# Optimization experiments

Hardware: AMD Instinct MI355X
Metric: run time of the kernel (lower is better)

Reference implementation:

```python
import jax, jax.numpy as jnp
import numpy as np

EPS = 1e-3  # keras LayerNormalization default epsilon


def layer_norm(x, gamma, beta):
    mean = jnp.mean(x, axis=-1, keepdims=True)
    var = jnp.var(x, axis=-1, keepdims=True)
    return (x - mean) * jax.lax.rsqrt(var + EPS) * gamma + beta


def setup_inputs() -> dict:
    key = jax.random.key(0)
    ks = jax.random.split(key, 4)
    B, H, W, C, Ci = 16, 64, 64, 512, 64
    return {
        "x": jax.random.normal(ks[0], (B, H, W, C), dtype=jnp.float32),
        "Wf": jax.random.normal(ks[1], (C, Ci), dtype=jnp.float32) * (1.0 / np.sqrt(C)),
        "Wh": jax.random.normal(ks[2], (C, Ci), dtype=jnp.float32) * (1.0 / np.sqrt(C)),
        "Wfgh": jax.random.normal(ks[3], (Ci, C), dtype=jnp.float32) * (1.0 / np.sqrt(Ci)),
        "gamma_f": jnp.ones((Ci,), jnp.float32),
        "beta_f": jnp.zeros((Ci,), jnp.float32),
        "gamma_h": jnp.ones((Ci,), jnp.float32),
        "beta_h": jnp.zeros((Ci,), jnp.float32),
        "gamma_fgh": jnp.ones((C,), jnp.float32),
        "beta_fgh": jnp.zeros((C,), jnp.float32),
        "scale": jnp.ones((1,), jnp.float32),
    }


def reference(x, Wf, Wh, Wfgh, gamma_f, beta_f, gamma_h, beta_h, gamma_fgh, beta_fgh, scale):
    # NOTE: original code uses w_f / LN_f for BOTH f and g branches (w_g unused).
    fg_base = layer_norm(jnp.einsum("bhwc,cd->bhwd", x, Wf), gamma_f, beta_f)  # [B,H,W,Ci]
    f = jnp.transpose(fg_base, (0, 2, 1, 3))  # Permute(2,1,3): swap H and W
    g = fg_base
    h = layer_norm(jnp.einsum("bhwc,cd->bhwd", x, Wh), gamma_h, beta_h)
    attn = jax.nn.softmax(f * g, axis=1)  # softmax over height axis
    out = jnp.einsum("bhwd,dc->bhwc", attn * h, Wfgh)
    out = layer_norm(out, gamma_fgh, beta_fgh)
    return out * scale + x
```

## Files before the change

### kernel.cpp

```cpp
#include <hip/hip_runtime.h>
#include <math.h>

#define BB 16
#define HH 64
#define WW 64
#define CC 512
#define CI 64
#define NROWS (BB * HH * WW)
#define LN_EPS 1e-3f

typedef __attribute__((ext_vector_type(8))) short bf16x8;
typedef __attribute__((ext_vector_type(4))) float f32x4;

__device__ __forceinline__ unsigned short f2bf(float f) {
  union {
    float f;
    unsigned int u;
  } v;
  v.f = f;
  unsigned int r = v.u + 0x7FFF + ((v.u >> 16) & 1);
  return (unsigned short)(r >> 16);
}

__device__ __forceinline__ float bf2f(unsigned short u) {
  union {
    unsigned int u;
    float f;
  } v;
  v.u = ((unsigned int)u) << 16;
  return v.f;
}

__device__ __forceinline__ unsigned int cvt_pk_bf16(float a, float b) {
  unsigned int r;
  asm("v_cvt_pk_bf16_f32 %0, %1, %2" : "=v"(r) : "v"(a), "v"(b));
  return r;
}

__device__ __forceinline__ void gload_lds16(const float* g, float* l) {
  __builtin_amdgcn_global_load_lds(
      (const __attribute__((address_space(1))) void*)g,
      (__attribute__((address_space(3))) void*)l, 16, 0, 0);
}

__global__ __launch_bounds__(256) void sgsa_prep(
    const float* __restrict__ Wf, const float* __restrict__ Wh,
    const float* __restrict__ Wo, unsigned short* __restrict__ WcT,
    unsigned short* __restrict__ WoT) {
  int tid = blockIdx.x * 256 + threadIdx.x;
  for (int i = tid; i < 128 * 512; i += gridDim.x * 256) {
    int col = i >> 9, k = i & 511;
    float v = (col < 64) ? Wf[k * 64 + col] : Wh[k * 64 + (col - 64)];
    WcT[i] = f2bf(v);
  }
  for (int i = tid; i < 512 * 64; i += gridDim.x * 256) {
    int col = i >> 6, k = i & 63;
    WoT[i] = f2bf(Wo[k * 512 + col]);
  }
}

__global__ __launch_bounds__(128) void sgsa_k1_mfma(
    const float* __restrict__ x, const unsigned short* __restrict__ WcT,
    const float* __restrict__ gf, const float* __restrict__ bf,
    const float* __restrict__ gh, const float* __restrict__ bh,
    float* __restrict__ fg, float* __restrict__ hl) {
  __shared__ float lds_a[2][64 * 64];

  const int tid = threadIdx.x;
  const int lane = tid & 63;
  const int wv = tid >> 6;
  const int cq = lane & 15;
  const int kg = lane >> 4;
  const int brow0 = blockIdx.x * 64;

  f32x4 acc[2][8];
#pragma unroll
  for (int rt = 0; rt < 2; ++rt)
#pragma unroll
    for (int ct = 0; ct < 8; ++ct) acc[rt][ct] = (f32x4){0.f, 0.f, 0.f, 0.f};

  int s_row[8], s_chk[8];
#pragma unroll
  for (int i = 0; i < 8; ++i) {
    int lin = (wv * 8 + i) * 64 + lane;
    s_row[i] = lin >> 4;
    s_chk[i] = (lin & 15) ^ ((lin >> 4) & 15);
  }

  auto stage = [&](int bufp, int ks) {
#pragma unroll
    for (int i = 0; i < 8; ++i) {
      const float* src =
          &x[(size_t)(brow0 + s_row[i]) * CC + ks * 64 + s_chk[i] * 4];
      gload_lds16(src, &lds_a[bufp][(wv * 8 + i) * 256]);
    }
  };

  stage(0, 0);
  __syncthreads();

  for (int ks = 0; ks < 8; ++ks) {
    const int bufp = ks & 1;
    if (ks < 7) stage(bufp ^ 1, ks + 1);

    const int kb0 = ks * 64;
#pragma unroll
    for (int kh = 0; kh < 2; ++kh) {
      const int kb2 = kh * 32;
      bf16x8 bfr[8];
#pragma unroll
      for (int ct = 0; ct < 8; ++ct)
        bfr[ct] =
            *(const bf16x8*)&WcT[(ct * 16 + cq) * 512 + kb0 + kb2 + kg * 8];
      union {
        bf16x8 v;
        unsigned int u[4];
      } af[2];
#pragma unroll
      for (int rt = 0; rt < 2; ++rt) {
        const int rl = wv * 32 + rt * 16 + cq;
        const int c0 = (kh * 8 + kg * 2) ^ cq;
        const int c1 = (kh * 8 + kg * 2 + 1) ^ cq;
        f32x4 a0 = *(const f32x4*)&lds_a[bufp][rl * 64 + c0 * 4];
        f32x4 a1 = *(const f32x4*)&lds_a[bufp][rl * 64 + c1 * 4];
        af[rt].u[0] = cvt_pk_bf16(a0[0], a0[1]);
        af[rt].u[1] = cvt_pk_bf16(a0[2], a0[3]);
        af[rt].u[2] = cvt_pk_bf16(a1[0], a1[1]);
        af[rt].u[3] = cvt_pk_bf16(a1[2], a1[3]);
      }
#pragma unroll
      for (int rt = 0; rt < 2; ++rt)
#pragma unroll
        for (int ct = 0; ct < 8; ++ct)
          acc[rt][ct] = __builtin_amdgcn_mfma_f32_16x16x32_bf16(
              af[rt].v, bfr[ct], acc[rt][ct], 0, 0, 0);
    }
    __syncthreads();
  }

  float gfv[4], bfv[4], ghv[4], bhv[4];
#pragma unroll
  for (int ct = 0; ct < 4; ++ct) {
    gfv[ct] = gf[ct * 16 + cq];
    bfv[ct] = bf[ct * 16 + cq];
    ghv[ct] = gh[ct * 16 + cq];
    bhv[ct] = bh[ct * 16 + cq];
  }

#pragma unroll
  for (int rt = 0; rt < 2; ++rt) {
#pragma unroll
    for (int r = 0; r < 4; ++r) {
      const int row = brow0 + wv * 32 + rt * 16 + kg * 4 + r;
      float s = acc[rt][0][r] + acc[rt][1][r] + acc[rt][2][r] + acc[rt][3][r];
      float q = acc[rt][0][r] * acc[rt][0][r] + acc[rt][1][r] * acc[rt][1][r] +
                acc[rt][2][r] * acc[rt][2][r] + acc[rt][3][r] * acc[rt][3][r];
#pragma unroll
      for (int m = 1; m < 16; m <<= 1) {
        s += __shfl_xor(s, m, 64);
        q += __shfl_xor(q, m, 64);
      }
      float mean = s * (1.f / 64.f);
      float var = q * (1.f / 64.f) - mean * mean;
      float inv = rsqrtf(var + LN_EPS);
#pragma unroll
      for (int ct = 0; ct < 4; ++ct) {
        float v = (acc[rt][ct][r] - mean) * inv * gfv[ct] + bfv[ct];
        fg[(size_t)row * CI + ct * 16 + cq] = v;
      }
      float s2 = acc[rt][4][r] + acc[rt][5][r] + acc[rt][6][r] + acc[rt][7][r];
      float q2 = acc[rt][4][r] * acc[rt][4][r] + acc[rt][5][r] * acc[rt][5][r] +
                 acc[rt][6][r] * acc[rt][6][r] + acc[rt][7][r] * acc[rt][7][r];
#pragma unroll
      for (int m = 1; m < 16; m <<= 1) {
        s2 += __shfl_xor(s2, m, 64);
        q2 += __shfl_xor(q2, m, 64);
      }
      float mean2 = s2 * (1.f / 64.f);
      float var2 = q2 * (1.f / 64.f) - mean2 * mean2;
      float inv2 = rsqrtf(var2 + LN_EPS);
#pragma unroll
      for (int ct = 0; ct < 4; ++ct) {
        float v = (acc[rt][ct + 4][r] - mean2) * inv2 * ghv[ct] + bhv[ct];
        hl[(size_t)row * CI + ct * 16 + cq] = v;
      }
    }
  }
}

__global__ __launch_bounds__(512, 2) void sgsa_k23(
    const float* __restrict__ fg, const float* __restrict__ hl,
    const unsigned short* __restrict__ WoT, const float* __restrict__ go,
    const float* __restrict__ bo, const float* __restrict__ scale,
    const float* __restrict__ x, float* __restrict__ out) {
  const int bid = (int)(blockIdx.x & 7) * 128 + (int)(blockIdx.x >> 3);
  const int b = bid >> 6;
  const int w = bid & 63;
  const int tid = threadIdx.x;
  const int lane = tid & 63;
  const int wv = tid >> 6;

  __shared__ float lds_f[64 * 64];
  __shared__ float lds_g[64 * 64];
  __shared__ float lds_h[64 * 64];
  __shared__ unsigned short t_hi[64 * 72];
  __shared__ unsigned short t_lo[64 * 72];
  __shared__ float red[8][64];
  __shared__ float s_red[8][32];
  __shared__ float q_red[8][32];

  const size_t base_g = ((size_t)(b * 64) * 64 + w) * 64;
  const size_t base_f = ((size_t)(b * 64 + w) * 64) * 64;

#pragma unroll
  for (int i = 0; i < 2; ++i) {
    const int c = (wv * 2 + i) * 64 + lane;
    const int grp = (wv * 2 + i) * 256;
    gload_lds16(&fg[base_f + (size_t)c * 4], &lds_f[grp]);
    const size_t soff = (size_t)(c >> 4) * 4096 + (c & 15) * 4;
    gload_lds16(&fg[base_g + soff], &lds_g[grp]);
    gload_lds16(&hl[base_g + soff], &lds_h[grp]);
  }
  __syncthreads();

  {
    const int d = tid & 63;
    const int q = tid >> 6;
    float sv[8];
    float ssum = 0.f;
#pragma unroll
    for (int i = 0; i < 8; ++i) {
      int h = q * 8 + i;
      sv[i] = __expf(lds_f[h * 64 + d] * lds_g[h * 64 + d]);
      ssum += sv[i];
    }
    red[q][d] = ssum;
    __syncthreads();
    ssum = 0.f;
#pragma unroll
    for (int j = 0; j < 8; ++j) ssum += red[j][d];
    float rinv = 1.f / ssum;

#pragma unroll
    for (int i = 0; i < 8; ++i) {
      int h = q * 8 + i;
      float t = sv[i] * rinv * lds_h[h * 64 + d];
      unsigned short th = f2bf(t);
      t_hi[h * 72 + d] = th;
      t_lo[h * 72 + d] = f2bf(t - bf2f(th));
    }
  }
  __syncthreads();

  const int rh = wv >> 2;
  const int cw = wv & 3;
  const int col0 = cw * 128;
  const int cq = lane & 15;
  const int kg = lane >> 4;
  const int trow0 = rh * 32;

  f32x4 acc[2][8];
#pragma unroll
  for (int rt = 0; rt < 2; ++rt)
#pragma unroll
    for (int ct = 0; ct < 8; ++ct) acc[rt][ct] = (f32x4){0.f, 0.f, 0.f, 0.f};

#pragma unroll
  for (int kk = 0; kk < 2; ++kk) {
    const int kb = kk * 32 + kg * 8;
    bf16x8 ah[2], al[2];
#pragma unroll
    for (int rt = 0; rt < 2; ++rt) {
      ah[rt] = *(const bf16x8*)&t_hi[(trow0 + rt * 16 + cq) * 72 + kb];
      al[rt] = *(const bf16x8*)&t_lo[(trow0 + rt * 16 + cq) * 72 + kb];
    }
#pragma unroll
    for (int half = 0; half < 2; ++half) {
      bf16x8 bfr[4];
#pragma unroll
      for (int c4 = 0; c4 < 4; ++c4) {
        const int ct = half * 4 + c4;
        bfr[c4] = *(const bf16x8*)&WoT[(col0 + ct * 16 + cq) * CI + kb];
      }
#pragma unroll
      for (int rt = 0; rt < 2; ++rt) {
#pragma unroll
        for (int c4 = 0; c4 < 4; ++c4) {
          const int ct = half * 4 + c4;
          acc[rt][ct] = __builtin_amdgcn_mfma_f32_16x16x32_bf16(
              ah[rt], bfr[c4], acc[rt][ct], 0, 0, 0);
          acc[rt][ct] = __builtin_amdgcn_mfma_f32_16x16x32_bf16(
              al[rt], bfr[c4], acc[rt][ct], 0, 0, 0);
        }
      }
    }
  }

#pragma unroll
  for (int rt = 0; rt < 2; ++rt) {
#pragma unroll
    for (int r = 0; r < 4; ++r) {
      float s = 0.f, qq = 0.f;
#pragma unroll
      for (int ct = 0; ct < 8; ++ct) {
        float v = acc[rt][ct][r];
        s += v;
        qq += v * v;
      }
#pragma unroll
      for (int m = 1; m < 16; m <<= 1) {
        s += __shfl_xor(s, m, 64);
        qq += __shfl_xor(qq, m, 64);
      }
      if (cq == 0) {
        s_red[wv][rt * 16 + kg * 4 + r] = s;
        q_red[wv][rt * 16 + kg * 4 + r] = qq;
      }
    }
  }

  float xv[2][4][8];
#pragma unroll
  for (int rt = 0; rt < 2; ++rt) {
#pragma unroll
    for (int r = 0; r < 4; ++r) {
      const int h = trow0 + rt * 16 + kg * 4 + r;
      const size_t base = (size_t)((b * 64 + h) * 64 + w) * CC;
#pragma unroll
      for (int ct = 0; ct < 8; ++ct)
        xv[rt][r][ct] = x[base + col0 + ct * 16 + cq];
    }
  }
  __syncthreads();

  const float sc = scale[0];
  float gov[8], bov[8];
#pragma unroll
  for (int ct = 0; ct < 8; ++ct) {
    gov[ct] = go[col0 + ct * 16 + cq];
    bov[ct] = bo[col0 + ct * 16 + cq];
  }

#pragma unroll
  for (int rt = 0; rt < 2; ++rt) {
#pragma unroll
    for (int r = 0; r < 4; ++r) {
      const int rl = rt * 16 + kg * 4 + r;
      const int h = trow0 + rl;
      float s = (s_red[rh * 4 + 0][rl] + s_red[rh * 4 + 1][rl]) +
                (s_red[rh * 4 + 2][rl] + s_red[rh * 4 + 3][rl]);
      float q = (q_red[rh * 4 + 0][rl] + q_red[rh * 4 + 1][rl]) +
                (q_red[rh * 4 + 2][rl] + q_red[rh * 4 + 3][rl]);
      float mean = s * (1.f / 512.f);
      float var = q * (1.f / 512.f) - mean * mean;
      float inv = rsqrtf(var + LN_EPS);
      const size_t base = (size_t)((b * 64 + h) * 64 + w) * CC;
#pragma unroll
      for (int ct = 0; ct < 8; ++ct) {
        const int col = col0 + ct * 16 + cq;
        float o = (acc[rt][ct][r] - mean) * inv * gov[ct] + bov[ct];
        out[base + col] = o * sc + xv[rt][r][ct];
      }
    }
  }
}

extern "C" void kernel_launch(void* const* d_in, const int* in_sizes, int n_in,
                              void* d_out, int out_size, void* d_ws,
                              size_t ws_size, hipStream_t stream) {
  const float* x = (const float*)d_in[0];
  const float* Wf = (const float*)d_in[1];
  const float* Wh = (const float*)d_in[2];
  const float* Wo = (const float*)d_in[3];
  const float* gf = (const float*)d_in[4];
  const float* bf = (const float*)d_in[5];
  const float* gh = (const float*)d_in[6];
  const float* bh = (const float*)d_in[7];
  const float* go = (const float*)d_in[8];
  const float* bo = (const float*)d_in[9];
  const float* sc = (const float*)d_in[10];
  float* out = (float*)d_out;

  unsigned short* WcT = (unsigned short*)d_ws;
  unsigned short* WoT = WcT + 128 * 512;
  float* fg = (float*)((char*)d_ws + (256 << 10));
  float* hl = fg + (size_t)NROWS * CI;

  sgsa_prep<<<128, 256, 0, stream>>>(Wf, Wh, Wo, WcT, WoT);
  sgsa_k1_mfma<<<NROWS / 64, 128, 0, stream>>>(x, WcT, gf, bf, gh, bh, fg, hl);
  sgsa_k23<<<BB * WW, 512, 0, stream>>>(fg, hl, WoT, go, bo, sc, x, out);
}
```

Measured before the change: 121.1 us.

## Split fused softmax+output GEMM kernel into separate softmax and GEMM kernels

The fused per-(b,w) kernel that did the height softmax, the output projection and the final LayerNorm is split in two. The first kernel computes the softmax-weighted h in place into the hl buffer using direct global loads. The second kernel is a row-contiguous 16-row-per-wave MFMA GEMM that does the full 512-column LayerNorm within one wave, with coalesced x/out access. This adds an extra global round trip of the 16 MB intermediate and another launch, in exchange for contiguous row access, no cross-wave LDS reductions and smaller blocks.

```diff
diff --git a/kernel.cpp b/kernel.cpp
--- a/kernel.cpp
+++ b/kernel.cpp
@@ -188,179 +188,121 @@
   }
 }
 
-__global__ __launch_bounds__(512, 2) void sgsa_k23(
-    const float* __restrict__ fg, const float* __restrict__ hl,
-    const unsigned short* __restrict__ WoT, const float* __restrict__ go,
-    const float* __restrict__ bo, const float* __restrict__ scale,
-    const float* __restrict__ x, float* __restrict__ out) {
+__global__ __launch_bounds__(512) void sgsa_k2(const float* __restrict__ fg,
+                                               float* __restrict__ hl) {
   const int bid = (int)(blockIdx.x & 7) * 128 + (int)(blockIdx.x >> 3);
   const int b = bid >> 6;
   const int w = bid & 63;
-  const int tid = threadIdx.x;
-  const int lane = tid & 63;
-  const int wv = tid >> 6;
-
-  __shared__ float lds_f[64 * 64];
-  __shared__ float lds_g[64 * 64];
-  __shared__ float lds_h[64 * 64];
-  __shared__ unsigned short t_hi[64 * 72];
-  __shared__ unsigned short t_lo[64 * 72];
+  const int d = threadIdx.x & 63;
+  const int q = threadIdx.x >> 6;
+
   __shared__ float red[8][64];
-  __shared__ float s_red[8][32];
-  __shared__ float q_red[8][32];
 
   const size_t base_g = ((size_t)(b * 64) * 64 + w) * 64;
   const size_t base_f = ((size_t)(b * 64 + w) * 64) * 64;
 
-#pragma unroll
-  for (int i = 0; i < 2; ++i) {
-    const int c = (wv * 2 + i) * 64 + lane;
-    const int grp = (wv * 2 + i) * 256;
-    gload_lds16(&fg[base_f + (size_t)c * 4], &lds_f[grp]);
-    const size_t soff = (size_t)(c >> 4) * 4096 + (c & 15) * 4;
-    gload_lds16(&fg[base_g + soff], &lds_g[grp]);
-    gload_lds16(&hl[base_g + soff], &lds_h[grp]);
-  }
+  float sv[8], hv[8];
+  float ssum = 0.f;
+#pragma unroll
+  for (int i = 0; i < 8; ++i) {
+    int h = q * 8 + i;
+    float g = fg[base_g + (size_t)h * 4096 + d];
+    float f = fg[base_f + (size_t)h * 64 + d];
+    hv[i] = hl[base_g + (size_t)h * 4096 + d];
+    sv[i] = __expf(f * g);
+    ssum += sv[i];
+  }
+  red[q][d] = ssum;
   __syncthreads();
-
-  {
-    const int d = tid & 63;
-    const int q = tid >> 6;
-    float sv[8];
-    float ssum = 0.f;
-#pragma unroll
-    for (int i = 0; i < 8; ++i) {
-      int h = q * 8 + i;
-      sv[i] = __expf(lds_f[h * 64 + d] * lds_g[h * 64 + d]);
-      ssum += sv[i];
-    }
-    red[q][d] = ssum;
-    __syncthreads();
-    ssum = 0.f;
-#pragma unroll
-    for (int j = 0; j < 8; ++j) ssum += red[j][d];
-    float rinv = 1.f / ssum;
-
-#pragma unroll
-    for (int i = 0; i < 8; ++i) {
-      int h = q * 8 + i;
-      float t = sv[i] * rinv * lds_h[h * 64 + d];
-      unsigned short th = f2bf(t);
-      t_hi[h * 72 + d] = th;
-      t_lo[h * 72 + d] = f2bf(t - bf2f(th));
-    }
-  }
-  __syncthreads();
-
-  const int rh = wv >> 2;
-  const int cw = wv & 3;
-  const int col0 = cw * 128;
+  ssum = 0.f;
+#pragma unroll
+  for (int j = 0; j < 8; ++j) ssum += red[j][d];
+  float rinv = 1.f / ssum;
+
+#pragma unroll
+  for (int i = 0; i < 8; ++i) {
+    int h = q * 8 + i;
+    hl[base_g + (size_t)h * 4096 + d] = sv[i] * rinv * hv[i];
+  }
+}
+
+__global__ __launch_bounds__(64) void sgsa_k3(
+    const float* __restrict__ t, const unsigned short* __restrict__ WoT,
+    const float* __restrict__ go, const float* __restrict__ bo,
+    const float* __restrict__ scale, const float* __restrict__ x,
+    float* __restrict__ out) {
+  const int lane = threadIdx.x;
   const int cq = lane & 15;
   const int kg = lane >> 4;
-  const int trow0 = rh * 32;
-
-  f32x4 acc[2][8];
-#pragma unroll
-  for (int rt = 0; rt < 2; ++rt)
-#pragma unroll
-    for (int ct = 0; ct < 8; ++ct) acc[rt][ct] = (f32x4){0.f, 0.f, 0.f, 0.f};
+  const int bid = (int)(blockIdx.x & 7) * 512 + (int)(blockIdx.x >> 3);
+  const int row0 = bid * 16;
+
+  bf16x8 ah[2], al[2];
+#pragma unroll
+  for (int kk = 0; kk < 2; ++kk) {
+    const float* ap = &t[(size_t)(row0 + cq) * CI + kk * 32 + kg * 8];
+    f32x4 a0 = *(const f32x4*)ap;
+    f32x4 a1 = *(const f32x4*)(ap + 4);
+#pragma unroll
+    for (int j = 0; j < 4; ++j) {
+      unsigned short h0 = f2bf(a0[j]);
+      unsigned short h1 = f2bf(a1[j]);
+      ah[kk][j] = (short)h0;
+      ah[kk][j + 4] = (short)h1;
+      al[kk][j] = (short)f2bf(a0[j] - bf2f(h0));
+      al[kk][j + 4] = (short)f2bf(a1[j] - bf2f(h1));
+    }
+  }
+
+  f32x4 acc[32];
+#pragma unroll
+  for (int ct = 0; ct < 32; ++ct) acc[ct] = (f32x4){0.f, 0.f, 0.f, 0.f};
 
 #pragma unroll
   for (int kk = 0; kk < 2; ++kk) {
     const int kb = kk * 32 + kg * 8;
-    bf16x8 ah[2], al[2];
-#pragma unroll
-    for (int rt = 0; rt < 2; ++rt) {
-      ah[rt] = *(const bf16x8*)&t_hi[(trow0 + rt * 16 + cq) * 72 + kb];
-      al[rt] = *(const bf16x8*)&t_lo[(trow0 + rt * 16 + cq) * 72 + kb];
-    }
-#pragma unroll
-    for (int half = 0; half < 2; ++half) {
-      bf16x8 bfr[4];
-#pragma unroll
-      for (int c4 = 0; c4 < 4; ++c4) {
-        const int ct = half * 4 + c4;
-        bfr[c4] = *(const bf16x8*)&WoT[(col0 + ct * 16 + cq) * CI + kb];
-      }
-#pragma unroll
-      for (int rt = 0; rt < 2; ++rt) {
-#pragma unroll
-        for (int c4 = 0; c4 < 4; ++c4) {
-          const int ct = half * 4 + c4;
-          acc[rt][ct] = __builtin_amdgcn_mfma_f32_16x16x32_bf16(
-              ah[rt], bfr[c4], acc[rt][ct], 0, 0, 0);
-          acc[rt][ct] = __builtin_amdgcn_mfma_f32_16x16x32_bf16(
-              al[rt], bfr[c4], acc[rt][ct], 0, 0, 0);
-        }
-      }
-    }
-  }
-
-#pragma unroll
-  for (int rt = 0; rt < 2; ++rt) {
-#pragma unroll
-    for (int r = 0; r < 4; ++r) {
-      float s = 0.f, qq = 0.f;
-#pragma unroll
-      for (int ct = 0; ct < 8; ++ct) {
-        float v = acc[rt][ct][r];
-        s += v;
-        qq += v * v;
-      }
-#pragma unroll
-      for (int m = 1; m < 16; m <<= 1) {
-        s += __shfl_xor(s, m, 64);
-        qq += __shfl_xor(qq, m, 64);
-      }
-      if (cq == 0) {
-        s_red[wv][rt * 16 + kg * 4 + r] = s;
-        q_red[wv][rt * 16 + kg * 4 + r] = qq;
-      }
-    }
-  }
-
-  float xv[2][4][8];
-#pragma unroll
-  for (int rt = 0; rt < 2; ++rt) {
-#pragma unroll
-    for (int r = 0; r < 4; ++r) {
-      const int h = trow0 + rt * 16 + kg * 4 + r;
-      const size_t base = (size_t)((b * 64 + h) * 64 + w) * CC;
-#pragma unroll
-      for (int ct = 0; ct < 8; ++ct)
-        xv[rt][r][ct] = x[base + col0 + ct * 16 + cq];
-    }
-  }
-  __syncthreads();
+#pragma unroll
+    for (int ct = 0; ct < 32; ++ct) {
+      bf16x8 bfr = *(const bf16x8*)&WoT[(ct * 16 + cq) * CI + kb];
+      acc[ct] =
+          __builtin_amdgcn_mfma_f32_16x16x32_bf16(ah[kk], bfr, acc[ct], 0, 0, 0);
+      acc[ct] =
+          __builtin_amdgcn_mfma_f32_16x16x32_bf16(al[kk], bfr, acc[ct], 0, 0, 0);
+    }
+  }
 
   const float sc = scale[0];
-  float gov[8], bov[8];
-#pragma unroll
-  for (int ct = 0; ct < 8; ++ct) {
-    gov[ct] = go[col0 + ct * 16 + cq];
-    bov[ct] = bo[col0 + ct * 16 + cq];
-  }
-
-#pragma unroll
-  for (int rt = 0; rt < 2; ++rt) {
-#pragma unroll
-    for (int r = 0; r < 4; ++r) {
-      const int rl = rt * 16 + kg * 4 + r;
-      const int h = trow0 + rl;
-      float s = (s_red[rh * 4 + 0][rl] + s_red[rh * 4 + 1][rl]) +
-                (s_red[rh * 4 + 2][rl] + s_red[rh * 4 + 3][rl]);
-      float q = (q_red[rh * 4 + 0][rl] + q_red[rh * 4 + 1][rl]) +
-                (q_red[rh * 4 + 2][rl] + q_red[rh * 4 + 3][rl]);
-      float mean = s * (1.f / 512.f);
-      float var = q * (1.f / 512.f) - mean * mean;
-      float inv = rsqrtf(var + LN_EPS);
-      const size_t base = (size_t)((b * 64 + h) * 64 + w) * CC;
-#pragma unroll
-      for (int ct = 0; ct < 8; ++ct) {
-        const int col = col0 + ct * 16 + cq;
-        float o = (acc[rt][ct][r] - mean) * inv * gov[ct] + bov[ct];
-        out[base + col] = o * sc + xv[rt][r][ct];
-      }
+
+#pragma unroll
+  for (int r = 0; r < 4; ++r) {
+    float s = 0.f, q = 0.f;
+#pragma unroll
+    for (int ct = 0; ct < 32; ++ct) {
+      float v = acc[ct][r];
+      s += v;
+      q += v * v;
+    }
+#pragma unroll
+    for (int m = 1; m < 16; m <<= 1) {
+      s += __shfl_xor(s, m, 64);
+      q += __shfl_xor(q, m, 64);
+    }
+    float mean = s * (1.f / 512.f);
+    float var = q * (1.f / 512.f) - mean * mean;
+    float inv = rsqrtf(var + LN_EPS);
+
+    const int row = row0 + kg * 4 + r;
+    const size_t base = (size_t)row * CC;
+
+    float xv[32];
+#pragma unroll
+    for (int ct = 0; ct < 32; ++ct) xv[ct] = x[base + ct * 16 + cq];
+
+#pragma unroll
+    for (int ct = 0; ct < 32; ++ct) {
+      const int col = ct * 16 + cq;
+      float o = (acc[ct][r] - mean) * inv * go[col] + bo[col];
+      out[base + col] = o * sc + xv[ct];
     }
   }
 }
@@ -388,5 +330,6 @@
 
   sgsa_prep<<<128, 256, 0, stream>>>(Wf, Wh, Wo, WcT, WoT);
   sgsa_k1_mfma<<<NROWS / 64, 128, 0, stream>>>(x, WcT, gf, bf, gh, bh, fg, hl);
-  sgsa_k23<<<BB * WW, 512, 0, stream>>>(fg, hl, WoT, go, bo, sc, x, out);
-}
+  sgsa_k2<<<BB * WW, 512, 0, stream>>>(fg, hl);
+  sgsa_k3<<<NROWS / 16, 64, 0, stream>>>(hl, WoT, go, bo, sc, x, out);
+}
```

Result: slower. 172.0 us (+42.1%).

## Shrink k23 to 256-thread blocks, drop LDS staging of f/g/h inputs

Applied to the files above, without the earlier changes.

The fused attention+projection kernel now runs 4 waves per block instead of 8. Each wave loads f, g and h straight from global memory into registers rather than staging them in LDS with async copies. The output GEMM is split into two 32-row passes per wave, and the residual x is read directly in the epilogue instead of being prefetched before the barrier. This cuts LDS use and raises the intended occupancy, at the cost of strided, uncoalesced global loads for g/h, serialized passes with extra barriers, and losing the early x prefetch.

```diff
diff --git a/kernel.cpp b/kernel.cpp
--- a/kernel.cpp
+++ b/kernel.cpp
@@ -188,7 +188,7 @@
   }
 }
 
-__global__ __launch_bounds__(512, 2) void sgsa_k23(
+__global__ __launch_bounds__(256, 4) void sgsa_k23(
     const float* __restrict__ fg, const float* __restrict__ hl,
     const unsigned short* __restrict__ WoT, const float* __restrict__ go,
     const float* __restrict__ bo, const float* __restrict__ scale,
@@ -200,51 +200,38 @@
   const int lane = tid & 63;
   const int wv = tid >> 6;
 
-  __shared__ float lds_f[64 * 64];
-  __shared__ float lds_g[64 * 64];
-  __shared__ float lds_h[64 * 64];
   __shared__ unsigned short t_hi[64 * 72];
   __shared__ unsigned short t_lo[64 * 72];
-  __shared__ float red[8][64];
-  __shared__ float s_red[8][32];
-  __shared__ float q_red[8][32];
+  __shared__ float red[4][64];
+  __shared__ float s_red[4][32];
+  __shared__ float q_red[4][32];
 
   const size_t base_g = ((size_t)(b * 64) * 64 + w) * 64;
   const size_t base_f = ((size_t)(b * 64 + w) * 64) * 64;
 
-#pragma unroll
-  for (int i = 0; i < 2; ++i) {
-    const int c = (wv * 2 + i) * 64 + lane;
-    const int grp = (wv * 2 + i) * 256;
-    gload_lds16(&fg[base_f + (size_t)c * 4], &lds_f[grp]);
-    const size_t soff = (size_t)(c >> 4) * 4096 + (c & 15) * 4;
-    gload_lds16(&fg[base_g + soff], &lds_g[grp]);
-    gload_lds16(&hl[base_g + soff], &lds_h[grp]);
-  }
-  __syncthreads();
-
   {
-    const int d = tid & 63;
-    const int q = tid >> 6;
-    float sv[8];
+    const int d = lane;
+    const int q = wv;
+    float sv[16], hv[16];
     float ssum = 0.f;
 #pragma unroll
-    for (int i = 0; i < 8; ++i) {
-      int h = q * 8 + i;
-      sv[i] = __expf(lds_f[h * 64 + d] * lds_g[h * 64 + d]);
+    for (int i = 0; i < 16; ++i) {
+      int h = q * 16 + i;
+      float g = fg[base_g + (size_t)h * 4096 + d];
+      float f = fg[base_f + (size_t)h * 64 + d];
+      hv[i] = hl[base_g + (size_t)h * 4096 + d];
+      sv[i] = __expf(f * g);
       ssum += sv[i];
     }
     red[q][d] = ssum;
     __syncthreads();
-    ssum = 0.f;
-#pragma unroll
-    for (int j = 0; j < 8; ++j) ssum += red[j][d];
+    ssum = (red[0][d] + red[1][d]) + (red[2][d] + red[3][d]);
     float rinv = 1.f / ssum;
 
 #pragma unroll
-    for (int i = 0; i < 8; ++i) {
-      int h = q * 8 + i;
-      float t = sv[i] * rinv * lds_h[h * 64 + d];
+    for (int i = 0; i < 16; ++i) {
+      int h = q * 16 + i;
+      float t = sv[i] * rinv * hv[i];
       unsigned short th = f2bf(t);
       t_hi[h * 72 + d] = th;
       t_lo[h * 72 + d] = f2bf(t - bf2f(th));
@@ -252,88 +239,11 @@
   }
   __syncthreads();
 
-  const int rh = wv >> 2;
-  const int cw = wv & 3;
-  const int col0 = cw * 128;
+  const int col0 = wv * 128;
   const int cq = lane & 15;
   const int kg = lane >> 4;
-  const int trow0 = rh * 32;
-
-  f32x4 acc[2][8];
-#pragma unroll
-  for (int rt = 0; rt < 2; ++rt)
-#pragma unroll
-    for (int ct = 0; ct < 8; ++ct) acc[rt][ct] = (f32x4){0.f, 0.f, 0.f, 0.f};
-
-#pragma unroll
-  for (int kk = 0; kk < 2; ++kk) {
-    const int kb = kk * 32 + kg * 8;
-    bf16x8 ah[2], al[2];
-#pragma unroll
-    for (int rt = 0; rt < 2; ++rt) {
-      ah[rt] = *(const bf16x8*)&t_hi[(trow0 + rt * 16 + cq) * 72 + kb];
-      al[rt] = *(const bf16x8*)&t_lo[(trow0 + rt * 16 + cq) * 72 + kb];
-    }
-#pragma unroll
-    for (int half = 0; half < 2; ++half) {
-      bf16x8 bfr[4];
-#pragma unroll
-      for (int c4 = 0; c4 < 4; ++c4) {
-        const int ct = half * 4 + c4;
-        bfr[c4] = *(const bf16x8*)&WoT[(col0 + ct * 16 + cq) * CI + kb];
-      }
-#pragma unroll
-      for (int rt = 0; rt < 2; ++rt) {
-#pragma unroll
-        for (int c4 = 0; c4 < 4; ++c4) {
-          const int ct = half * 4 + c4;
-          acc[rt][ct] = __builtin_amdgcn_mfma_f32_16x16x32_bf16(
-              ah[rt], bfr[c4], acc[rt][ct], 0, 0, 0);
-          acc[rt][ct] = __builtin_amdgcn_mfma_f32_16x16x32_bf16(
-              al[rt], bfr[c4], acc[rt][ct], 0, 0, 0);
-        }
-      }
-    }
-  }
-
-#pragma unroll
-  for (int rt = 0; rt < 2; ++rt) {
-#pragma unroll
-    for (int r = 0; r < 4; ++r) {
-      float s = 0.f, qq = 0.f;
-#pragma unroll
-      for (int ct = 0; ct < 8; ++ct) {
-        float v = acc[rt][ct][r];
-        s += v;
-        qq += v * v;
-      }
-#pragma unroll
-      for (int m = 1; m < 16; m <<= 1) {
-        s += __shfl_xor(s, m, 64);
-        qq += __shfl_xor(qq, m, 64);
-      }
-      if (cq == 0) {
-        s_red[wv][rt * 16 + kg * 4 + r] = s;
-        q_red[wv][rt * 16 + kg * 4 + r] = qq;
-      }
-    }
-  }
-
-  float xv[2][4][8];
-#pragma unroll
-  for (int rt = 0; rt < 2; ++rt) {
-#pragma unroll
-    for (int r = 0; r < 4; ++r) {
-      const int h = trow0 + rt * 16 + kg * 4 + r;
-      const size_t base = (size_t)((b * 64 + h) * 64 + w) * CC;
-#pragma unroll
-      for (int ct = 0; ct < 8; ++ct)
-        xv[rt][r][ct] = x[base + col0 + ct * 16 + cq];
-    }
-  }
-  __syncthreads();
-
   const float sc = scale[0];
+
   float gov[8], bov[8];
 #pragma unroll
   for (int ct = 0; ct < 8; ++ct) {
@@ -341,27 +251,92 @@
     bov[ct] = bo[col0 + ct * 16 + cq];
   }
 
-#pragma unroll
-  for (int rt = 0; rt < 2; ++rt) {
-#pragma unroll
-    for (int r = 0; r < 4; ++r) {
-      const int rl = rt * 16 + kg * 4 + r;
-      const int h = trow0 + rl;
-      float s = (s_red[rh * 4 + 0][rl] + s_red[rh * 4 + 1][rl]) +
-                (s_red[rh * 4 + 2][rl] + s_red[rh * 4 + 3][rl]);
-      float q = (q_red[rh * 4 + 0][rl] + q_red[rh * 4 + 1][rl]) +
-                (q_red[rh * 4 + 2][rl] + q_red[rh * 4 + 3][rl]);
-      float mean = s * (1.f / 512.f);
-      float var = q * (1.f / 512.f) - mean * mean;
-      float inv = rsqrtf(var + LN_EPS);
-      const size_t base = (size_t)((b * 64 + h) * 64 + w) * CC;
-#pragma unroll
-      for (int ct = 0; ct < 8; ++ct) {
-        const int col = col0 + ct * 16 + cq;
-        float o = (acc[rt][ct][r] - mean) * inv * gov[ct] + bov[ct];
-        out[base + col] = o * sc + xv[rt][r][ct];
-      }
-    }
+#pragma unroll 1
+  for (int pass = 0; pass < 2; ++pass) {
+    const int trow0 = pass * 32;
+
+    f32x4 acc[2][8];
+#pragma unroll
+    for (int rt = 0; rt < 2; ++rt)
+#pragma unroll
+      for (int ct = 0; ct < 8; ++ct) acc[rt][ct] = (f32x4){0.f, 0.f, 0.f, 0.f};
+
+#pragma unroll
+    for (int kk = 0; kk < 2; ++kk) {
+      const int kb = kk * 32 + kg * 8;
+      bf16x8 ah[2], al[2];
+#pragma unroll
+      for (int rt = 0; rt < 2; ++rt) {
+        ah[rt] = *(const bf16x8*)&t_hi[(trow0 + rt * 16 + cq) * 72 + kb];
+        al[rt] = *(const bf16x8*)&t_lo[(trow0 + rt * 16 + cq) * 72 + kb];
+      }
+#pragma unroll
+      for (int half = 0; half < 2; ++half) {
+        bf16x8 bfr[4];
+#pragma unroll
+        for (int c4 = 0; c4 < 4; ++c4) {
+          const int ct = half * 4 + c4;
+          bfr[c4] = *(const bf16x8*)&WoT[(col0 + ct * 16 + cq) * CI + kb];
+        }
+#pragma unroll
+        for (int rt = 0; rt < 2; ++rt) {
+#pragma unroll
+          for (int c4 = 0; c4 < 4; ++c4) {
+            const int ct = half * 4 + c4;
+            acc[rt][ct] = __builtin_amdgcn_mfma_f32_16x16x32_bf16(
+                ah[rt], bfr[c4], acc[rt][ct], 0, 0, 0);
+            acc[rt][ct] = __builtin_amdgcn_mfma_f32_16x16x32_bf16(
+                al[rt], bfr[c4], acc[rt][ct], 0, 0, 0);
+          }
+        }
+      }
+    }
+
+#pragma unroll
+    for (int rt = 0; rt < 2; ++rt) {
+#pragma unroll
+      for (int r = 0; r < 4; ++r) {
+        float s = 0.f, qq = 0.f;
+#pragma unroll
+        for (int ct = 0; ct < 8; ++ct) {
+          float v = acc[rt][ct][r];
+          s += v;
+          qq += v * v;
+        }
+#pragma unroll
+        for (int m = 1; m < 16; m <<= 1) {
+          s += __shfl_xor(s, m, 64);
+          qq += __shfl_xor(qq, m, 64);
+        }
+        if (cq == 0) {
+          s_red[wv][rt * 16 + kg * 4 + r] = s;
+          q_red[wv][rt * 16 + kg * 4 + r] = qq;
+        }
+      }
+    }
+    __syncthreads();
+
+#pragma unroll
+    for (int rt = 0; rt < 2; ++rt) {
+#pragma unroll
+      for (int r = 0; r < 4; ++r) {
+        const int rl = rt * 16 + kg * 4 + r;
+        const int h = trow0 + rl;
+        float s = (s_red[0][rl] + s_red[1][rl]) + (s_red[2][rl] + s_red[3][rl]);
+        float q = (q_red[0][rl] + q_red[1][rl]) + (q_red[2][rl] + q_red[3][rl]);
+        float mean = s * (1.f / 512.f);
+        float var = q * (1.f / 512.f) - mean * mean;
+        float inv = rsqrtf(var + LN_EPS);
+        const size_t base = (size_t)((b * 64 + h) * 64 + w) * CC;
+#pragma unroll
+        for (int ct = 0; ct < 8; ++ct) {
+          const int col = col0 + ct * 16 + cq;
+          float o = (acc[rt][ct][r] - mean) * inv * gov[ct] + bov[ct];
+          out[base + col] = o * sc + x[base + col];
+        }
+      }
+    }
+    if (pass == 0) __syncthreads();
   }
 }
 
@@ -388,5 +363,5 @@
 
   sgsa_prep<<<128, 256, 0, stream>>>(Wf, Wh, Wo, WcT, WoT);
   sgsa_k1_mfma<<<NROWS / 64, 128, 0, stream>>>(x, WcT, gf, bf, gh, bh, fg, hl);
-  sgsa_k23<<<BB * WW, 512, 0, stream>>>(fg, hl, WoT, go, bo, sc, x, out);
-}
+  sgsa_k23<<<BB * WW, 256, 0, stream>>>(fg, hl, WoT, go, bo, sc, x, out);
+}
```

Result: slower. 175.0 us (+44.5%).
